# Kernel optimization log

Measured on AMD Instinct MI355X. Metric: run time of the kernel, lower is better.

## Reference

```python
import jax, jax.numpy as jnp
import numpy as np

# Model dims (match init_kwargs)
L = 2048; B = 2; E = 1024; H = 16; NUM = 2; NG = 4; DG = 16
ODIM = E // H // NUM        # 32  origin_head_dim
DQK = ODIM * NG             # 128 qk_head_dim
QKD = DQK * H               # 2048 qk_dim
DV = E // H                 # 64  v_head_dim
EPS = 1e-12


def _one_mask(n, e, n_groups, step):
    """Faithful port of MultiheadSpluAttention.get_one_mask (numpy, setup-time only)."""
    e1 = e * n_groups
    mask = np.ones((n, e1))
    row_num = (e1 - e) // step + 1
    group1 = [list(range(i * step, i * step + e)) for i in range(row_num)]
    group2 = group1[::-1]
    group_index = [group1, group2]
    col_index = []
    l = n // row_num
    k = 0
    for i in range(l):
        for j in range(i * row_num, (i + 1) * row_num):
            col_index.append(group_index[k][j % row_num])
        k = 1 - k
    if n % row_num != 0:
        for j in range(l * row_num, n):
            col_index.append(group_index[k][j % row_num])
    mask[np.arange(n).reshape(-1, 1), np.array(col_index)] = 0
    return mask


def _build_masks(n):
    # head 0: no mask; heads 1..H-1 use step = head index
    ms = [np.zeros((n, DQK))]
    for s in range(1, H):
        ms.append(_one_mask(n, ODIM, NG, s))
    masks = np.stack(ms).astype(bool)            # (H, n, DQK); True = zero-out
    gmask = np.ones((n, DQK), dtype=bool)        # global: keep only first/last DG rows
    gmask[:DG, :] = False
    gmask[n - DG:, :] = False
    return jnp.asarray(masks), jnp.asarray(gmask)


def _xavier(key, shape, gain=1.0):
    fan_out, fan_in = shape
    a = gain * np.sqrt(6.0 / (fan_in + fan_out))
    return jax.random.uniform(key, shape, jnp.float32, -a, a)


def setup_inputs() -> dict:
    key = jax.random.key(0)
    ks = jax.random.split(key, 8)
    g = 1.0 / np.sqrt(2.0)
    masks, gmask = _build_masks(L)
    return {
        "query": jax.random.normal(ks[0], (L, B, E), jnp.float32),
        "key": jax.random.normal(ks[1], (L, B, E), jnp.float32),
        "value": jax.random.normal(ks[2], (L, B, E), jnp.float32),
        "Wq": _xavier(ks[3], (QKD, E), g), "bq": jnp.zeros((QKD,), jnp.float32),
        "Wk": _xavier(ks[4], (QKD, E), g), "bk": jnp.zeros((QKD,), jnp.float32),
        "Wv": _xavier(ks[5], (E, E), g),  "bv": jnp.zeros((E,), jnp.float32),
        "Wo": _xavier(ks[6], (E, E)),     "bo": jnp.zeros((E,), jnp.float32),
        "masks": masks,   # (H, L, DQK) bool
        "gmask": gmask,   # (L, DQK) bool
    }


def reference(query, key, value, Wq, bq, Wk, bk, Wv, bv, Wo, bo, masks, gmask):
    Lq, Bb, Ee = query.shape
    S = key.shape[0]
    Hh, _, dqk = masks.shape
    dv = Ee // Hh
    scaling = float(Wq.shape[0]) ** (-0.5)  # qk_dim ** -0.5

    q = jax.nn.relu(query @ Wq.T + bq) * scaling          # (L, B, QKD)
    k = jax.nn.relu(key @ Wk.T + bk)                       # (S, B, QKD)
    v = value @ Wv.T + bv                                  # (S, B, E)

    q = q.reshape(Lq, Bb, Hh, dqk).transpose(1, 2, 0, 3)   # (B, H, L, dqk)
    k = k.reshape(S, Bb, Hh, dqk).transpose(1, 2, 0, 3)    # (B, H, S, dqk)
    v = v.reshape(S, Bb, Hh, dv).transpose(1, 2, 0, 3)     # (B, H, S, dv)

    q1 = jnp.where(masks[None, :, :Lq], 0.0, q)            # per-head group mask
    k1 = jnp.where(masks[None, :, :S], 0.0, k)
    kg = jnp.where(gmask[None, None, :S], 0.0, k)          # keep only global tokens

    w = (jnp.einsum('bhld,bhsd->bhls', q1, k1)
         + jnp.einsum('bhld,bhsd->bhls', q, kg))           # (B, H, L, S)
    denom = jnp.maximum(jnp.sum(w, axis=-1, keepdims=True), EPS)
    w = w / denom                                          # relu-linear normalization

    out = jnp.einsum('bhls,bhsd->bhld', w, v)              # (B, H, L, dv)
    out = out.transpose(2, 0, 1, 3).reshape(Lq, Bb, Ee)    # (L, B, E)
    return out @ Wo.T + bo
```

## Files before the change

### kernel.cpp

```cpp
#include <hip/hip_runtime.h>

typedef unsigned short u16;
typedef __attribute__((ext_vector_type(8))) short s16x8;
typedef __attribute__((ext_vector_type(4))) float f32x4;

#define DEV static __device__ __forceinline__

#define CB 2
#define CM 4096
#define MBH 16640
#define OQ 0u
#define OK 4194304u
#define OV 8388608u
#define OWQ 12582912u
#define OWK 14680064u
#define OWV 16777216u
#define OWO 17825792u
#define SCALING 0.022097086912079608f

DEV float b2f(u16 u) { union { unsigned int i; float f; } x; x.i = (unsigned int)u << 16; return x.f; }
DEV u16 f2b(float f) {
  union { float f; unsigned int i; } x; x.f = f;
  unsigned int r = (x.i + 0x7FFFu + ((x.i >> 16) & 1u)) >> 16;
  return (u16)r;
}

DEV void async_cp16(const u16* g, u16* l) {
  __builtin_amdgcn_global_load_lds((__attribute__((address_space(1))) void*)g,
                                   (__attribute__((address_space(3))) void*)l,
                                   16, 0, 0);
}

#define MFMA16 __builtin_amdgcn_mfma_f32_16x16x32_bf16

__global__ void detect_stride(const unsigned char* __restrict__ m, int* __restrict__ flag) {
  if (threadIdx.x == 0) {
    const size_t base = (size_t)1 * 2048 * 128;
    int shift = 0;
    const int cands[3] = {0, 2, 3};
    for (int t = 0; t < 3; ++t) {
      int s = cands[t];
      bool ok = (m[(base + 100) << s] == 1) && (m[(base + 10) << s] == 0) &&
                (m[(base + 32) << s] == 1) && (m[(base + 31) << s] == 0);
      if (ok) { shift = s; break; }
    }
    *flag = shift;
  }
}

struct ConvDesc { const float* src; unsigned dst_off; unsigned n; };
struct ConvArgs { ConvDesc d[7]; };

__global__ __launch_bounds__(256) void convert_all(ConvArgs a, u16* __restrict__ dst_base) {
  ConvDesc dd = a.d[blockIdx.y];
  unsigned i = (blockIdx.x * 256u + threadIdx.x) * 4u;
  if (i >= dd.n) return;
  float4 v = *(const float4*)(dd.src + i);
  ushort4 p;
  p.x = f2b(v.x); p.y = f2b(v.y); p.z = f2b(v.z); p.w = f2b(v.w);
  *(ushort4*)(dst_base + dd.dst_off + i) = p;
}

__global__ __launch_bounds__(256) void gemm_qkv(const u16* __restrict__ cvt,
                                                const float* __restrict__ bq,
                                                const float* __restrict__ bk,
                                                const float* __restrict__ bv,
                                                u16* __restrict__ qbuf,
                                                u16* __restrict__ kbuf,
                                                u16* __restrict__ vbuf,
                                                u16* __restrict__ kg,
                                                const unsigned char* __restrict__ mb,
                                                const int* __restrict__ flag) {
  __shared__ u16 sA[128 * 32];
  __shared__ u16 sB[128 * 32];
  const int bx = blockIdx.x;

  const u16* A; const u16* W; const float* bias; u16* C;
  int N, nx; bool relu, domask; float scale;
  if (bx < 16) {
    A = cvt + OQ; W = cvt + OWQ; bias = bq; C = qbuf;
    N = 2048; nx = bx; relu = true; domask = false; scale = SCALING;
  } else if (bx < 32) {
    A = cvt + OK; W = cvt + OWK; bias = bk; C = kbuf;
    N = 2048; nx = bx - 16; relu = true; domask = true; scale = 1.0f;
  } else {
    A = cvt + OV; W = cvt + OWV; bias = bv; C = vbuf;
    N = 1024; nx = bx - 32; relu = false; domask = false; scale = 1.0f;
  }

  const int tid = threadIdx.x;
  const int lane = tid & 63;
  const int wv = tid >> 6;
  const int m0 = blockIdx.y * 128;
  const int n0 = nx * 128;

  const int rowi = lane >> 2;
  const int chk = lane & 3;
  const int lr = lane & 15;
  const int lq = lane >> 4;
  const int mq = (wv >> 1) * 64;
  const int nq = (wv & 1) * 64;

  const int shift = domask ? *flag : 0;

  f32x4 acc[4][4] = {};

  for (int k0 = 0; k0 < 1024; k0 += 32) {
#pragma unroll
    for (int i = 0; i < 2; ++i) {
      int t = wv * 2 + i;
      int row = t * 16 + rowi;
      async_cp16(A + (size_t)(m0 + row) * 1024 + k0 + chk * 8, sA + t * 512);
      async_cp16(W + (size_t)(n0 + row) * 1024 + k0 + chk * 8, sB + t * 512);
    }
    __syncthreads();
    s16x8 af[4], bfr[4];
#pragma unroll
    for (int mt = 0; mt < 4; ++mt)
      af[mt] = *(const s16x8*)&sA[(mq + mt * 16 + lr) * 32 + lq * 8];
#pragma unroll
    for (int nt = 0; nt < 4; ++nt)
      bfr[nt] = *(const s16x8*)&sB[(nq + nt * 16 + lr) * 32 + lq * 8];
#pragma unroll
    for (int mt = 0; mt < 4; ++mt)
#pragma unroll
      for (int nt = 0; nt < 4; ++nt)
        acc[mt][nt] = MFMA16(af[mt], bfr[nt], acc[mt][nt], 0, 0, 0);
    __syncthreads();
  }

#pragma unroll
  for (int mt = 0; mt < 4; ++mt) {
#pragma unroll
    for (int nt = 0; nt < 4; ++nt) {
      int col = n0 + nq + nt * 16 + lr;
      float bv_ = bias[col];
      size_t mcb = (size_t)(col >> 7) * 262144 + (col & 127);
#pragma unroll
      for (int r = 0; r < 4; ++r) {
        int row = m0 + mq + mt * 16 + lq * 4 + r;
        float x = acc[mt][nt][r] + bv_;
        if (relu) x = fmaxf(x, 0.0f);
        x *= scale;
        u16 vb = f2b(x);
        if (domask) {
          int s = row >> 1;
          u16 out = mb[(mcb + (size_t)s * 128) << shift] ? (u16)0 : vb;
          C[(size_t)row * N + col] = out;
          if (s < 16 || s >= 2032) {
            int gi = s < 16 ? s : s - 2016;
            kg[(size_t)((gi << 1) | (row & 1)) * 2048 + col] = vb;
          }
        } else {
          C[(size_t)row * N + col] = vb;
        }
      }
    }
  }
}

__global__ __launch_bounds__(256) void gemm_bt_f32(const u16* __restrict__ A,
                                                   const u16* __restrict__ W,
                                                   const float* __restrict__ bias,
                                                   float* __restrict__ Cp,
                                                   int M, int N, int K) {
  __shared__ u16 sA[128 * 32];
  __shared__ u16 sB[128 * 32];
  const int tid = threadIdx.x;
  const int lane = tid & 63;
  const int wv = tid >> 6;
  const int m0 = blockIdx.y * 128;
  const int n0 = blockIdx.x * 128;

  const int rowi = lane >> 2;
  const int chk = lane & 3;
  const int lr = lane & 15;
  const int lq = lane >> 4;
  const int mq = (wv >> 1) * 64;
  const int nq = (wv & 1) * 64;

  f32x4 acc[4][4] = {};

  for (int k0 = 0; k0 < K; k0 += 32) {
#pragma unroll
    for (int i = 0; i < 2; ++i) {
      int t = wv * 2 + i;
      int row = t * 16 + rowi;
      async_cp16(A + (size_t)(m0 + row) * K + k0 + chk * 8, sA + t * 512);
      async_cp16(W + (size_t)(n0 + row) * K + k0 + chk * 8, sB + t * 512);
    }
    __syncthreads();
    s16x8 af[4], bfr[4];
#pragma unroll
    for (int mt = 0; mt < 4; ++mt)
      af[mt] = *(const s16x8*)&sA[(mq + mt * 16 + lr) * 32 + lq * 8];
#pragma unroll
    for (int nt = 0; nt < 4; ++nt)
      bfr[nt] = *(const s16x8*)&sB[(nq + nt * 16 + lr) * 32 + lq * 8];
#pragma unroll
    for (int mt = 0; mt < 4; ++mt)
#pragma unroll
      for (int nt = 0; nt < 4; ++nt)
        acc[mt][nt] = MFMA16(af[mt], bfr[nt], acc[mt][nt], 0, 0, 0);
    __syncthreads();
  }

#pragma unroll
  for (int mt = 0; mt < 4; ++mt) {
#pragma unroll
    for (int nt = 0; nt < 4; ++nt) {
      int col = n0 + nq + nt * 16 + lr;
      float bv = bias[col];
#pragma unroll
      for (int r = 0; r < 4; ++r) {
        int row = m0 + mq + mt * 16 + lq * 4 + r;
        Cp[(size_t)row * N + col] = acc[mt][nt][r] + bv;
      }
    }
  }
}

__global__ __launch_bounds__(256) void build_m_mfma(const u16* __restrict__ kbuf,
                                                    const u16* __restrict__ vbuf,
                                                    const u16* __restrict__ kgbuf,
                                                    float* __restrict__ Mbuf) {
  __shared__ u16 sKr[32 * 128];
  __shared__ u16 sVr[32 * 64];
  const int tid = threadIdx.x;
  const int lane = tid & 63;
  const int wv = tid >> 6;
  const int lr = lane & 15;
  const int lq = lane >> 4;
  const int chunk = blockIdx.x;
  const int bh = blockIdx.y;
  const int b = bh >> 4, h = bh & 15;

  const int sA = wv * 4 + (lane >> 4);
  const int dA = (lane & 15) * 8;
  const int sV = wv * 8 + (lane >> 3);
  const int eV = (lane & 7) * 8;
  u16* dstK1 = sKr + wv * 512;
  u16* dstK2 = sKr + 2048 + wv * 512;
  u16* dstV = sVr + wv * 512;

  const s16x8 onesf = {0x3F80, 0x3F80, 0x3F80, 0x3F80, 0x3F80, 0x3F80, 0x3F80, 0x3F80};

  f32x4 acc[2][4] = {};
  f32x4 accm[2] = {};

  for (int ks = 0; ks < 8; ++ks) {
    const int s0 = chunk * 256 + ks * 32;
    async_cp16(kbuf + (size_t)((s0 + sA) * 2 + b) * 2048 + h * 128 + dA, dstK1);
    async_cp16(kbuf + (size_t)((s0 + 16 + sA) * 2 + b) * 2048 + h * 128 + dA, dstK2);
    async_cp16(vbuf + (size_t)((s0 + sV) * 2 + b) * 1024 + h * 64 + eV, dstV);
    __syncthreads();
    s16x8 A0, A1, B0, B1, B2, B3;
#pragma unroll
    for (int j = 0; j < 8; ++j) {
      const int sr = (lq * 8 + j) * 128;
      A0[j] = (short)sKr[sr + wv * 32 + lr];
      A1[j] = (short)sKr[sr + wv * 32 + 16 + lr];
      const int vr = (lq * 8 + j) * 64;
      B0[j] = (short)sVr[vr + lr];
      B1[j] = (short)sVr[vr + 16 + lr];
      B2[j] = (short)sVr[vr + 32 + lr];
      B3[j] = (short)sVr[vr + 48 + lr];
    }
    acc[0][0] = MFMA16(A0, B0, acc[0][0], 0, 0, 0);
    acc[0][1] = MFMA16(A0, B1, acc[0][1], 0, 0, 0);
    acc[0][2] = MFMA16(A0, B2, acc[0][2], 0, 0, 0);
    acc[0][3] = MFMA16(A0, B3, acc[0][3], 0, 0, 0);
    acc[1][0] = MFMA16(A1, B0, acc[1][0], 0, 0, 0);
    acc[1][1] = MFMA16(A1, B1, acc[1][1], 0, 0, 0);
    acc[1][2] = MFMA16(A1, B2, acc[1][2], 0, 0, 0);
    acc[1][3] = MFMA16(A1, B3, acc[1][3], 0, 0, 0);
    accm[0] = MFMA16(A0, onesf, accm[0], 0, 0, 0);
    accm[1] = MFMA16(A1, onesf, accm[1], 0, 0, 0);
    __syncthreads();
  }

  float* Mg = Mbuf + (size_t)bh * MBH;
#pragma unroll
  for (int dg = 0; dg < 2; ++dg) {
    const int dbase = wv * 32 + dg * 16 + lq * 4;
#pragma unroll
    for (int eg = 0; eg < 4; ++eg)
#pragma unroll
      for (int r = 0; r < 4; ++r)
        atomicAdd(&Mg[(size_t)(dbase + r) * 64 + eg * 16 + lr], acc[dg][eg][r]);
    if (lr == 0) {
#pragma unroll
      for (int r = 0; r < 4; ++r) atomicAdd(&Mg[16384 + dbase + r], accm[dg][r]);
    }
  }

  if (chunk == 0) {
    f32x4 acc2[2][4] = {};
    f32x4 accm2[2] = {};
    const int sVact = sV < 16 ? sV : 2016 + sV;
    async_cp16(kgbuf + (size_t)(sA * 2 + b) * 2048 + h * 128 + dA, dstK1);
    async_cp16(kgbuf + (size_t)((16 + sA) * 2 + b) * 2048 + h * 128 + dA, dstK2);
    async_cp16(vbuf + (size_t)(sVact * 2 + b) * 1024 + h * 64 + eV, dstV);
    __syncthreads();
    s16x8 A0, A1, B0, B1, B2, B3;
#pragma unroll
    for (int j = 0; j < 8; ++j) {
      const int sr = (lq * 8 + j) * 128;
      A0[j] = (short)sKr[sr + wv * 32 + lr];
      A1[j] = (short)sKr[sr + wv * 32 + 16 + lr];
      const int vr = (lq * 8 + j) * 64;
      B0[j] = (short)sVr[vr + lr];
      B1[j] = (short)sVr[vr + 16 + lr];
      B2[j] = (short)sVr[vr + 32 + lr];
      B3[j] = (short)sVr[vr + 48 + lr];
    }
    acc2[0][0] = MFMA16(A0, B0, acc2[0][0], 0, 0, 0);
    acc2[0][1] = MFMA16(A0, B1, acc2[0][1], 0, 0, 0);
    acc2[0][2] = MFMA16(A0, B2, acc2[0][2], 0, 0, 0);
    acc2[0][3] = MFMA16(A0, B3, acc2[0][3], 0, 0, 0);
    acc2[1][0] = MFMA16(A1, B0, acc2[1][0], 0, 0, 0);
    acc2[1][1] = MFMA16(A1, B1, acc2[1][1], 0, 0, 0);
    acc2[1][2] = MFMA16(A1, B2, acc2[1][2], 0, 0, 0);
    acc2[1][3] = MFMA16(A1, B3, acc2[1][3], 0, 0, 0);
    accm2[0] = MFMA16(A0, onesf, accm2[0], 0, 0, 0);
    accm2[1] = MFMA16(A1, onesf, accm2[1], 0, 0, 0);
#pragma unroll
    for (int dg = 0; dg < 2; ++dg) {
      const int dbase = wv * 32 + dg * 16 + lq * 4;
#pragma unroll
      for (int eg = 0; eg < 4; ++eg)
#pragma unroll
        for (int r = 0; r < 4; ++r)
          Mg[8192 + (size_t)(dbase + r) * 64 + eg * 16 + lr] = acc2[dg][eg][r];
      if (lr == 0) {
#pragma unroll
        for (int r = 0; r < 4; ++r) Mg[16512 + dbase + r] = accm2[dg][r];
      }
    }
  }
}

__global__ __launch_bounds__(256) void apply_f32(const u16* __restrict__ qbuf,
                                                 const float* __restrict__ Mbuf,
                                                 u16* __restrict__ attn,
                                                 const unsigned char* __restrict__ mbytes,
                                                 const int* __restrict__ flag) {
  __shared__ float sM1[32 * 64];
  __shared__ float sM2[32 * 64];
  __shared__ float sm1[32], sm2[32];
  const int bh = blockIdx.x;
  const int b = bh >> 4, h = bh & 15;
  const int ll = threadIdx.x >> 2;
  const int eg = threadIdx.x & 3;
  const int l = blockIdx.y * 64 + ll;
  const float* Mg = Mbuf + (size_t)bh * MBH;
  const u16* qr = qbuf + ((size_t)(l * CB + b)) * 2048 + h * 128;
  const int shift = *flag;
  const size_t mrow = ((size_t)h * 2048 + l) * 128;

  float acc[16] = {};
  float den = 0.f;

  for (int c = 0; c < 4; ++c) {
    __syncthreads();
    {
      int base = threadIdx.x * 8;
      *(float4*)&sM1[base] = *(const float4*)&Mg[c * 2048 + base];
      *(float4*)&sM1[base + 4] = *(const float4*)&Mg[c * 2048 + base + 4];
      *(float4*)&sM2[base] = *(const float4*)&Mg[8192 + c * 2048 + base];
      *(float4*)&sM2[base + 4] = *(const float4*)&Mg[8192 + c * 2048 + base + 4];
      if (threadIdx.x < 32) sm1[threadIdx.x] = Mg[16384 + c * 32 + threadIdx.x];
      else if (threadIdx.x < 64) sm2[threadIdx.x - 32] = Mg[16512 + c * 32 + threadIdx.x - 32];
    }
    __syncthreads();
    for (int j = 0; j < 32; ++j) {
      int d = c * 32 + j;
      float qd = b2f(qr[d]);
      float q1d = mbytes[(mrow + d) << shift] ? 0.f : qd;
      den += q1d * sm1[j] + qd * sm2[j];
      const float* r1 = &sM1[j * 64 + eg * 16];
      const float* r2 = &sM2[j * 64 + eg * 16];
#pragma unroll
      for (int e = 0; e < 4; ++e) {
        float4 a = *(const float4*)&r1[e * 4];
        float4 bb = *(const float4*)&r2[e * 4];
        acc[e * 4 + 0] += q1d * a.x + qd * bb.x;
        acc[e * 4 + 1] += q1d * a.y + qd * bb.y;
        acc[e * 4 + 2] += q1d * a.z + qd * bb.z;
        acc[e * 4 + 3] += q1d * a.w + qd * bb.w;
      }
    }
  }

  float inv = 1.0f / fmaxf(den, 1e-12f);
  u16* o = attn + ((size_t)(l * CB + b)) * 1024 + h * 64 + eg * 16;
#pragma unroll
  for (int g = 0; g < 2; ++g) {
    ushort4 pk;
    pk.x = f2b(acc[g * 8 + 0] * inv);
    pk.y = f2b(acc[g * 8 + 1] * inv);
    pk.z = f2b(acc[g * 8 + 2] * inv);
    pk.w = f2b(acc[g * 8 + 3] * inv);
    ushort4 pk2;
    pk2.x = f2b(acc[g * 8 + 4] * inv);
    pk2.y = f2b(acc[g * 8 + 5] * inv);
    pk2.z = f2b(acc[g * 8 + 6] * inv);
    pk2.w = f2b(acc[g * 8 + 7] * inv);
    *(ushort4*)&o[g * 8] = pk;
    *(ushort4*)&o[g * 8 + 4] = pk2;
  }
}

extern "C" void kernel_launch(void* const* d_in, const int* in_sizes, int n_in,
                              void* d_out, int out_size, void* d_ws, size_t ws_size,
                              hipStream_t stream) {
  (void)in_sizes; (void)n_in; (void)out_size; (void)ws_size;

  const float* bq = (const float*)d_in[4];
  const float* bk = (const float*)d_in[6];
  const float* bv = (const float*)d_in[8];
  const float* bo = (const float*)d_in[10];
  const unsigned char* mbytes = (const unsigned char*)d_in[11];

  char* ws = (char*)d_ws;
  u16* qbuf = (u16*)ws;
  u16* kbuf = (u16*)(ws + 16777216);
  float* Mbuf = (float*)(ws + 33554432);
  int* flag = (int*)(ws + 35684352);
  u16* cvt = (u16*)(ws + 35684368);
  u16* vbuf = (u16*)d_out;
  u16* kgbuf = (u16*)((char*)d_out + 8388608);
  u16* attn = kbuf;

  hipMemsetAsync(Mbuf, 0, 32 * MBH * sizeof(float), stream);
  detect_stride<<<dim3(1), dim3(64), 0, stream>>>(mbytes, flag);

  ConvArgs ca;
  ca.d[0] = {(const float*)d_in[0], OQ, 4194304u};
  ca.d[1] = {(const float*)d_in[1], OK, 4194304u};
  ca.d[2] = {(const float*)d_in[2], OV, 4194304u};
  ca.d[3] = {(const float*)d_in[3], OWQ, 2097152u};
  ca.d[4] = {(const float*)d_in[5], OWK, 2097152u};
  ca.d[5] = {(const float*)d_in[7], OWV, 1048576u};
  ca.d[6] = {(const float*)d_in[9], OWO, 1048576u};
  convert_all<<<dim3(4096, 7), dim3(256), 0, stream>>>(ca, cvt);

  dim3 blk(256);
  gemm_qkv<<<dim3(40, 32), blk, 0, stream>>>(cvt, bq, bk, bv, qbuf, kbuf, vbuf, kgbuf, mbytes, flag);
  build_m_mfma<<<dim3(8, 32), blk, 0, stream>>>(kbuf, vbuf, kgbuf, Mbuf);
  apply_f32<<<dim3(32, 32), blk, 0, stream>>>(qbuf, Mbuf, attn, mbytes, flag);
  gemm_bt_f32<<<dim3(8, 32), blk, 0, stream>>>(attn, cvt + OWO, bo, (float*)d_out, CM, 1024, 1024);
}
```

Baseline: 375.3 us.

## Move attention apply step to bf16 MFMA with hi/lo split of M matrices

Replaces the scalar fp32 apply kernel with an MFMA-based kernel that computes q1·M1 + q·M2 (plus a denominator column) using bf16 matrix cores. A new prep kernel splits each fp32 M entry into high and low bf16 parts and stores them transposed with an XOR swizzle, so the MFMA kernel can load them into LDS asynchronously without bank conflicts. The split keeps close to fp32 accuracy at the cost of four MFMAs per tile and an extra small kernel launch. The prepared matrices are written into the output buffer, reusing space that vbuf/kgbuf held earlier.

```diff
diff --git a/kernel.cpp b/kernel.cpp
--- a/kernel.cpp
+++ b/kernel.cpp
@@ -340,74 +340,103 @@
   }
 }
 
-__global__ __launch_bounds__(256) void apply_f32(const u16* __restrict__ qbuf,
-                                                 const float* __restrict__ Mbuf,
-                                                 u16* __restrict__ attn,
-                                                 const unsigned char* __restrict__ mbytes,
-                                                 const int* __restrict__ flag) {
-  __shared__ float sM1[32 * 64];
-  __shared__ float sM2[32 * 64];
-  __shared__ float sm1[32], sm2[32];
+__global__ __launch_bounds__(128) void prep_m(const float* __restrict__ Mbuf,
+                                              u16* __restrict__ Mp) {
+  const int n = blockIdx.x;
+  const int bh = blockIdx.y;
+  const int d = threadIdx.x;
+  const float* Mg = Mbuf + (size_t)bh * MBH;
+  float v1 = 0.f, v2 = 0.f;
+  if (n < 64) { v1 = Mg[d * 64 + n]; v2 = Mg[8192 + d * 64 + n]; }
+  else if (n == 64) { v1 = Mg[16384 + d]; v2 = Mg[16512 + d]; }
+  u16 h1 = f2b(v1); float l1 = v1 - b2f(h1);
+  u16 h2 = f2b(v2); float l2 = v2 - b2f(h2);
+  u16* dst = Mp + (size_t)bh * 40960;
+  const int dsw = d ^ ((n & 7) << 3);
+  dst[(0 * 80 + n) * 128 + dsw] = h1;
+  dst[(1 * 80 + n) * 128 + dsw] = f2b(l1);
+  dst[(2 * 80 + n) * 128 + dsw] = h2;
+  dst[(3 * 80 + n) * 128 + dsw] = f2b(l2);
+}
+
+__global__ __launch_bounds__(256) void apply_mfma(const u16* __restrict__ qbuf,
+                                                  const u16* __restrict__ Mp,
+                                                  u16* __restrict__ attn,
+                                                  const unsigned char* __restrict__ mb,
+                                                  const int* __restrict__ flag) {
+  __shared__ u16 sB[4 * 80 * 128];
+  const int tid = threadIdx.x;
+  const int lane = tid & 63;
+  const int wv = tid >> 6;
+  const int lr = lane & 15;
+  const int lq = lane >> 4;
   const int bh = blockIdx.x;
   const int b = bh >> 4, h = bh & 15;
-  const int ll = threadIdx.x >> 2;
-  const int eg = threadIdx.x & 3;
-  const int l = blockIdx.y * 64 + ll;
-  const float* Mg = Mbuf + (size_t)bh * MBH;
-  const u16* qr = qbuf + ((size_t)(l * CB + b)) * 2048 + h * 128;
+  const int l0 = blockIdx.y * 256;
   const int shift = *flag;
-  const size_t mrow = ((size_t)h * 2048 + l) * 128;
-
-  float acc[16] = {};
-  float den = 0.f;
-
-  for (int c = 0; c < 4; ++c) {
-    __syncthreads();
-    {
-      int base = threadIdx.x * 8;
-      *(float4*)&sM1[base] = *(const float4*)&Mg[c * 2048 + base];
-      *(float4*)&sM1[base + 4] = *(const float4*)&Mg[c * 2048 + base + 4];
-      *(float4*)&sM2[base] = *(const float4*)&Mg[8192 + c * 2048 + base];
-      *(float4*)&sM2[base + 4] = *(const float4*)&Mg[8192 + c * 2048 + base + 4];
-      if (threadIdx.x < 32) sm1[threadIdx.x] = Mg[16384 + c * 32 + threadIdx.x];
-      else if (threadIdx.x < 64) sm2[threadIdx.x - 32] = Mg[16512 + c * 32 + threadIdx.x - 32];
-    }
-    __syncthreads();
-    for (int j = 0; j < 32; ++j) {
-      int d = c * 32 + j;
-      float qd = b2f(qr[d]);
-      float q1d = mbytes[(mrow + d) << shift] ? 0.f : qd;
-      den += q1d * sm1[j] + qd * sm2[j];
-      const float* r1 = &sM1[j * 64 + eg * 16];
-      const float* r2 = &sM2[j * 64 + eg * 16];
-#pragma unroll
-      for (int e = 0; e < 4; ++e) {
-        float4 a = *(const float4*)&r1[e * 4];
-        float4 bb = *(const float4*)&r2[e * 4];
-        acc[e * 4 + 0] += q1d * a.x + qd * bb.x;
-        acc[e * 4 + 1] += q1d * a.y + qd * bb.y;
-        acc[e * 4 + 2] += q1d * a.z + qd * bb.z;
-        acc[e * 4 + 3] += q1d * a.w + qd * bb.w;
+
+  {
+    const u16* src = Mp + (size_t)bh * 40960;
+#pragma unroll
+    for (int i = 0; i < 20; ++i)
+      async_cp16(src + (size_t)(i * 4 + wv) * 512 + lane * 8, sB + (i * 4 + wv) * 512);
+  }
+  __syncthreads();
+
+  f32x4 acc[4][5] = {};
+  const int lrow = l0 + wv * 64;
+
+  for (int d0 = 0; d0 < 128; d0 += 32) {
+    s16x8 aq[4], a1[4];
+#pragma unroll
+    for (int mt = 0; mt < 4; ++mt) {
+      const int l = lrow + mt * 16 + lr;
+      aq[mt] = *(const s16x8*)&qbuf[((size_t)(l * 2 + b)) * 2048 + h * 128 + d0 + lq * 8];
+      const size_t mi = ((size_t)(h * 2048 + l)) * 128 + d0 + lq * 8;
+      s16x8 t = aq[mt];
+      if (shift == 0) {
+        unsigned long long mm = *(const unsigned long long*)&mb[mi];
+#pragma unroll
+        for (int j = 0; j < 8; ++j)
+          if ((mm >> (8 * j)) & 0xffull) t[j] = 0;
+      } else {
+#pragma unroll
+        for (int j = 0; j < 8; ++j)
+          if (mb[(mi + j) << shift]) t[j] = 0;
       }
-    }
-  }
-
-  float inv = 1.0f / fmaxf(den, 1e-12f);
-  u16* o = attn + ((size_t)(l * CB + b)) * 1024 + h * 64 + eg * 16;
-#pragma unroll
-  for (int g = 0; g < 2; ++g) {
-    ushort4 pk;
-    pk.x = f2b(acc[g * 8 + 0] * inv);
-    pk.y = f2b(acc[g * 8 + 1] * inv);
-    pk.z = f2b(acc[g * 8 + 2] * inv);
-    pk.w = f2b(acc[g * 8 + 3] * inv);
-    ushort4 pk2;
-    pk2.x = f2b(acc[g * 8 + 4] * inv);
-    pk2.y = f2b(acc[g * 8 + 5] * inv);
-    pk2.z = f2b(acc[g * 8 + 6] * inv);
-    pk2.w = f2b(acc[g * 8 + 7] * inv);
-    *(ushort4*)&o[g * 8] = pk;
-    *(ushort4*)&o[g * 8 + 4] = pk2;
+      a1[mt] = t;
+    }
+    const int eb = (d0 >> 3) + lq;
+#pragma unroll
+    for (int nt = 0; nt < 5; ++nt) {
+      const int n = nt * 16 + lr;
+      const u16* bp = &sB[(size_t)n * 128 + ((eb ^ (n & 7)) << 3)];
+      s16x8 b1h = *(const s16x8*)&bp[0];
+      s16x8 b1l = *(const s16x8*)&bp[10240];
+      s16x8 b2h = *(const s16x8*)&bp[20480];
+      s16x8 b2l = *(const s16x8*)&bp[30720];
+#pragma unroll
+      for (int mt = 0; mt < 4; ++mt) {
+        acc[mt][nt] = MFMA16(a1[mt], b1h, acc[mt][nt], 0, 0, 0);
+        acc[mt][nt] = MFMA16(a1[mt], b1l, acc[mt][nt], 0, 0, 0);
+        acc[mt][nt] = MFMA16(aq[mt], b2h, acc[mt][nt], 0, 0, 0);
+        acc[mt][nt] = MFMA16(aq[mt], b2l, acc[mt][nt], 0, 0, 0);
+      }
+    }
+  }
+
+#pragma unroll
+  for (int mt = 0; mt < 4; ++mt) {
+#pragma unroll
+    for (int r = 0; r < 4; ++r) {
+      float den = __shfl(acc[mt][4][r], lane & 48);
+      float inv = 1.0f / fmaxf(den, 1e-12f);
+      const int row = lrow + mt * 16 + lq * 4 + r;
+      u16* o = attn + ((size_t)(row * 2 + b)) * 1024 + h * 64;
+#pragma unroll
+      for (int nt = 0; nt < 4; ++nt)
+        o[nt * 16 + lr] = f2b(acc[mt][nt][r] * inv);
+    }
   }
 }
 
@@ -430,6 +459,7 @@
   u16* cvt = (u16*)(ws + 35684368);
   u16* vbuf = (u16*)d_out;
   u16* kgbuf = (u16*)((char*)d_out + 8388608);
+  u16* Mprep = (u16*)d_out;
   u16* attn = kbuf;
 
   hipMemsetAsync(Mbuf, 0, 32 * MBH * sizeof(float), stream);
@@ -448,6 +478,7 @@
   dim3 blk(256);
   gemm_qkv<<<dim3(40, 32), blk, 0, stream>>>(cvt, bq, bk, bv, qbuf, kbuf, vbuf, kgbuf, mbytes, flag);
   build_m_mfma<<<dim3(8, 32), blk, 0, stream>>>(kbuf, vbuf, kgbuf, Mbuf);
-  apply_f32<<<dim3(32, 32), blk, 0, stream>>>(qbuf, Mbuf, attn, mbytes, flag);
+  prep_m<<<dim3(80, 32), dim3(128), 0, stream>>>(Mbuf, Mprep);
+  apply_mfma<<<dim3(32, 8), blk, 0, stream>>>(qbuf, Mprep, attn, mbytes, flag);
   gemm_bt_f32<<<dim3(8, 32), blk, 0, stream>>>(attn, cvt + OWO, bo, (float*)d_out, CM, 1024, 1024);
 }
```

After: 354.1 us. -5.6%, faster.
